# Optimization experiments

Hardware: AMD Instinct MI355X
Metric: run time of the kernel (lower is better)

## Reference

```python
import jax, jax.numpy as jnp
import numpy as np

B, S, D, H = 2, 2048, 1024, 16
HD = D // H  # head_dim = 64
NEG = -1.0e9


def setup_inputs() -> dict:
    key = jax.random.key(0)
    ks = jax.random.split(key, 9)
    s = 1.0 / np.sqrt(D)
    return {
        "x": jax.random.normal(ks[0], (B, S, D), jnp.float32),
        "mask": jnp.ones((B, S), jnp.float32),
        "Wq": jax.random.normal(ks[1], (D, D), jnp.float32) * s,
        "bq": jnp.zeros((D,), jnp.float32),
        "Wk": jax.random.normal(ks[2], (D, D), jnp.float32) * s,
        "bk": jnp.zeros((D,), jnp.float32),
        "Wv": jax.random.normal(ks[3], (D, D), jnp.float32) * s,
        "bv": jnp.zeros((D,), jnp.float32),
        "Wo": jax.random.normal(ks[4], (D, D), jnp.float32) * s,
        "bo": jnp.zeros((D,), jnp.float32),
    }


def reference(x, mask, Wq, bq, Wk, bk, Wv, bv, Wo, bo):
    # QKV projections -> [B, H, S, HD]
    def proj(t, W, b):
        return (t @ W + b).reshape(B, S, H, HD).transpose(0, 2, 1, 3)

    q = proj(x, Wq, bq)
    k = proj(x, Wk, bk)
    v = proj(x, Wv, bv)

    scores = jnp.einsum("bhqd,bhkd->bhqk", q, k) / jnp.sqrt(jnp.asarray(HD, x.dtype))
    # causal mask: scores * m + (1-m) * -1e9 (matches original exactly)
    cm = jnp.tril(jnp.ones((S, S), x.dtype))[None, None]
    scores = scores * cm + (1.0 - cm) * NEG
    # 2D padding mask branch
    scores = scores + (1.0 - mask[:, None, None, :]) * NEG

    attn = jax.nn.softmax(scores, axis=-1)
    out = jnp.einsum("bhqk,bhkd->bqhd", attn, v).reshape(B, S, D)
    return out @ Wo + bo
```

## Files before the change

kernel.cpp:

```cpp
#include <hip/hip_runtime.h>
#include <hip/hip_bf16.h>
#include <cstdint>
#include <cstddef>

typedef __attribute__((ext_vector_type(8))) short short8;
typedef __attribute__((ext_vector_type(4))) float floatx4;
typedef __attribute__((ext_vector_type(2))) unsigned int uintx2;

#define MFMA16(a, b, c) __builtin_amdgcn_mfma_f32_16x16x32_bf16((a), (b), (c), 0, 0, 0)
#define LOG2E 1.44269504088896340736f
#define EXP2(x) __builtin_amdgcn_exp2f(x)

__device__ __forceinline__ unsigned short f2bf(float f) {
  unsigned int u = __builtin_bit_cast(unsigned int, f);
  u += 0x7fffu + ((u >> 16) & 1u);
  return (unsigned short)(u >> 16);
}

__device__ __forceinline__ unsigned int pk2(float a, float b) {
  float2 f; f.x = a; f.y = b;
  __hip_bfloat162 h = __float22bfloat162_rn(f);
  unsigned int u;
  __builtin_memcpy(&u, &h, 4);
  return u;
}

typedef __attribute__((address_space(1))) void gvoid_t;
typedef __attribute__((address_space(3))) void svoid_t;
__device__ __forceinline__ void gload_lds16(const void* g, void* l) {
  __builtin_amdgcn_global_load_lds((gvoid_t*)(uintptr_t)g, (svoid_t*)(uintptr_t)l, 16, 0, 0);
}

__global__ void convert_x(const float* __restrict__ x, unsigned short* __restrict__ xb) {
  int i = (blockIdx.x * 256 + threadIdx.x) * 4;
  floatx4 v = *(const floatx4*)(x + i);
  uintx2 o;
  o[0] = pk2(v[0], v[1]);
  o[1] = pk2(v[2], v[3]);
  *(uintx2*)(xb + i) = o;
}

__global__ void transpose_w(const float* __restrict__ Wq, const float* __restrict__ Wk,
                            const float* __restrict__ Wv, const float* __restrict__ Wo,
                            unsigned short* __restrict__ Wqkvt, unsigned short* __restrict__ Wot) {
  __shared__ float tile[32][33];
  int z = blockIdx.z;
  const float* W = (z == 0) ? Wq : (z == 1) ? Wk : (z == 2) ? Wv : Wo;
  unsigned short* out = (z == 3) ? Wot : (Wqkvt + (size_t)z * 1024 * 1024);
  int n0 = blockIdx.x * 32, k0 = blockIdx.y * 32;
  int tx = threadIdx.x, ty = threadIdx.y;
#pragma unroll
  for (int j = 0; j < 4; ++j)
    tile[ty + j * 8][tx] = W[(size_t)(k0 + ty + j * 8) * 1024 + n0 + tx];
  __syncthreads();
#pragma unroll
  for (int j = 0; j < 4; ++j)
    out[(size_t)(n0 + ty + j * 8) * 1024 + k0 + tx] = f2bf(tile[tx][ty + j * 8]);
}

#define GEMM_PROLOGUE()                                                        \
  __shared__ __align__(16) unsigned short As[128 * 64];                        \
  __shared__ __align__(16) unsigned short Bs[128 * 64];                        \
  const int tid = threadIdx.x;                                                 \
  const int lane = tid & 63;                                                   \
  const int wid = tid >> 6;                                                    \
  const int col = lane & 15;                                                   \
  const int quad = lane >> 4;                                                  \
  const int m0 = blockIdx.x * 128;                                             \
  const int n0 = blockIdx.y * 128;                                             \
  const int wm = wid >> 1;                                                     \
  const int wn = wid & 1;                                                      \
  floatx4 acc[4][4];                                                           \
  _Pragma("unroll") for (int i = 0; i < 4; ++i)                                \
      _Pragma("unroll") for (int j = 0; j < 4; ++j)                            \
          acc[i][j] = (floatx4)(0.f);                                          \
  _Pragma("unroll 1") for (int kt = 0; kt < 16; ++kt) {                        \
    __syncthreads();                                                           \
    _Pragma("unroll") for (int call = 0; call < 4; ++call) {                   \
      int c = call * 256 + tid;                                                \
      int r = c >> 3, ch = c & 7;                                              \
      gload_lds16(A + (size_t)(m0 + r) * 1024 + kt * 64 + ((ch ^ (r & 7)) * 8),\
                  As + (size_t)(call * 256 + wid * 64) * 8);                   \
      gload_lds16(Bt + (size_t)(n0 + r) * 1024 + kt * 64 + ((ch ^ (r & 7)) * 8),\
                  Bs + (size_t)(call * 256 + wid * 64) * 8);                   \
    }                                                                          \
    __syncthreads();                                                           \
    _Pragma("unroll") for (int ks = 0; ks < 2; ++ks) {                         \
      short8 af[4], bf[4];                                                     \
      _Pragma("unroll") for (int rt = 0; rt < 4; ++rt) {                       \
        int row = wm * 64 + rt * 16 + col;                                     \
        af[rt] = *(const short8*)&As[row * 64 + (((ks * 4 + quad) ^ (row & 7)) * 8)]; \
      }                                                                        \
      _Pragma("unroll") for (int ct = 0; ct < 4; ++ct) {                       \
        int row = wn * 64 + ct * 16 + col;                                     \
        bf[ct] = *(const short8*)&Bs[row * 64 + (((ks * 4 + quad) ^ (row & 7)) * 8)]; \
      }                                                                        \
      _Pragma("unroll") for (int rt = 0; rt < 4; ++rt)                         \
          _Pragma("unroll") for (int ct = 0; ct < 4; ++ct)                     \
              acc[rt][ct] = MFMA16(af[rt], bf[ct], acc[rt][ct]);               \
    }                                                                          \
  }

__global__ __launch_bounds__(256, 3)
void gemm_qkv(const unsigned short* __restrict__ A, const unsigned short* __restrict__ Bt,
              const float* __restrict__ bq, const float* __restrict__ bk,
              const float* __restrict__ bv,
              unsigned short* __restrict__ Qo, unsigned short* __restrict__ Ko,
              unsigned short* __restrict__ Vo) {
  GEMM_PROLOGUE()
  const int nseg = n0 >> 10;
  const float* bias = (nseg == 0) ? bq : ((nseg == 1) ? bk : bv);
#pragma unroll
  for (int rt = 0; rt < 4; ++rt) {
#pragma unroll
    for (int ct = 0; ct < 4; ++ct) {
      int mg = m0 + wm * 64 + rt * 16 + quad * 4;
      int ng = n0 + wn * 64 + ct * 16 + col;
      int c = ng & 1023;
      int hh = c >> 6, hd = c & 63;
      int b_ = mg >> 11, s = mg & 2047;
      float bb = bias[c];
      if (nseg == 2) {
        uintx2 pk;
        pk[0] = pk2(acc[rt][ct][0] + bb, acc[rt][ct][1] + bb);
        pk[1] = pk2(acc[rt][ct][2] + bb, acc[rt][ct][3] + bb);
        *(uintx2*)&Vo[(size_t)(b_ * 16 + hh) * 131072 + (size_t)hd * 2048 + s] = pk;
      } else {
        unsigned short* dst =
            ((nseg == 0) ? Qo : Ko) + ((size_t)(b_ * 16 + hh) * 2048 + s) * 64 + hd;
        float scl = (nseg == 0) ? (0.125f * LOG2E) : 1.0f;
#pragma unroll
        for (int i = 0; i < 4; ++i) dst[(size_t)i * 64] = f2bf((acc[rt][ct][i] + bb) * scl);
      }
    }
  }
}

__global__ __launch_bounds__(256, 3)
void gemm_out(const unsigned short* __restrict__ A, const unsigned short* __restrict__ Bt,
              const float* __restrict__ bo, float* __restrict__ Out) {
  GEMM_PROLOGUE()
#pragma unroll
  for (int rt = 0; rt < 4; ++rt) {
#pragma unroll
    for (int ct = 0; ct < 4; ++ct) {
      int mg = m0 + wm * 64 + rt * 16 + quad * 4;
      int ng = n0 + wn * 64 + ct * 16 + col;
      float bb = bo[ng];
#pragma unroll
      for (int i = 0; i < 4; ++i)
        Out[(size_t)(mg + i) * 1024 + ng] = acc[rt][ct][i] + bb;
    }
  }
}

__global__ __launch_bounds__(256, 4)
void flash_attn(const unsigned short* __restrict__ Q, const unsigned short* __restrict__ K,
                const unsigned short* __restrict__ Vt, const float* __restrict__ mask,
                unsigned short* __restrict__ O) {
  __shared__ __align__(16) unsigned short Ks[128 * 64];
  __shared__ __align__(16) unsigned short Vs[64 * 128];

  const int tid = threadIdx.x;
  const int lane = tid & 63;
  const int wid = tid >> 6;
  const int col = lane & 15;
  const int quad = lane >> 4;
  const int slot = (int)(blockIdx.x >> 8);
  const int g = (int)(blockIdx.x & 255);
  const int h8 = g >> 5;
  const int bh = g & 31;
  const int j = (slot == 0) ? (31 - h8) : (slot == 1) ? h8 : (slot == 2) ? (23 - h8) : (8 + h8);
  const int b = bh >> 4, h = bh & 15;
  const int q0 = j * 64;
  const int tdiag = j >> 1;

  const unsigned short* Qp = Q + (size_t)bh * 2048 * 64;
  const unsigned short* Kp = K + (size_t)bh * 2048 * 64;
  const unsigned short* Vp = Vt + (size_t)bh * 64 * 2048;
  const float* mp = mask + b * 2048;

  const int lr8 = lane >> 3, lc8 = lane & 7;
  const int lr16 = lane >> 4, lc16 = lane & 15;
  const floatx4 fzero = (floatx4)(0.f);
  const floatx4 fone = (floatx4)(1.f);

#pragma unroll
  for (int i = 0; i < 2; ++i) {
    int seg = wid * 2 + i;
    int r = seg * 8 + lr8;
    gload_lds16(Qp + (size_t)(q0 + r) * 64 + ((lc8 ^ (r & 7)) * 8), Ks + seg * 512);
  }
  __syncthreads();
  short8 qf[2];
  {
    int q = wid * 16 + col;
#pragma unroll
    for (int ks = 0; ks < 2; ++ks)
      qf[ks] = *(const short8*)&Ks[q * 64 + (((ks * 4 + quad) ^ (q & 7)) * 8)];
  }
  unsigned int mbits = 0;
  for (int t = 0; t <= tdiag; ++t) {
    float2 mv = *(const float2*)&mp[t * 128 + lane * 2];
    unsigned long long bb = __ballot(mv.x != 1.f || mv.y != 1.f);
    mbits |= (bb ? 1u : 0u) << t;
  }

  floatx4 o[4];
#pragma unroll
  for (int dt = 0; dt < 4; ++dt) o[dt] = fzero;
  float mrow = -1e30f;
  float lrow = 0.f;

#pragma unroll 1
  for (int t = 0; t <= tdiag; ++t) {
    __syncthreads();
#pragma unroll
    for (int i = 0; i < 4; ++i) {
      int seg = wid * 4 + i;
      int r = seg * 8 + lr8;
      gload_lds16(Kp + (size_t)(t * 128 + r) * 64 + ((lc8 ^ (r & 7)) * 8), Ks + seg * 512);
    }
#pragma unroll
    for (int i = 0; i < 4; ++i) {
      int seg = wid * 4 + i;
      int r = seg * 4 + lr16;
      gload_lds16(Vp + (size_t)r * 2048 + t * 128 + ((lc16 ^ (r & 15)) * 8), Vs + seg * 512);
    }
    __syncthreads();

    floatx4 sc[8];
    __builtin_amdgcn_s_setprio(1);
#pragma unroll
    for (int rt = 0; rt < 8; ++rt) {
      int kr = rt * 16 + col;
      short8 kf0 = *(const short8*)&Ks[kr * 64 + ((quad ^ (col & 7)) * 8)];
      short8 kf1 = *(const short8*)&Ks[kr * 64 + (((4 + quad) ^ (col & 7)) * 8)];
      floatx4 s0 = MFMA16(kf0, qf[0], fzero);
      sc[rt] = MFMA16(kf1, qf[1], s0);
    }
    __builtin_amdgcn_s_setprio(0);
    __syncthreads();

    if (__builtin_amdgcn_readfirstlane(mbits >> t) & 1) {
#pragma unroll
      for (int rt = 0; rt < 8; ++rt) {
        floatx4 mm = *(const floatx4*)&mp[t * 128 + rt * 16 + quad * 4];
        sc[rt] += (fone - mm) * (-1.0e9f * LOG2E);
      }
    }
    if (t == tdiag) {
      int qg = q0 + wid * 16 + col;
#pragma unroll
      for (int rt = 0; rt < 8; ++rt)
#pragma unroll
        for (int i = 0; i < 4; ++i)
          if (t * 128 + rt * 16 + quad * 4 + i > qg) sc[rt][i] = -1.0e9f * LOG2E;
    }

    float mt = -1e30f;
#pragma unroll
    for (int rt = 0; rt < 8; ++rt)
      mt = fmaxf(mt, fmaxf(fmaxf(sc[rt][0], sc[rt][1]), fmaxf(sc[rt][2], sc[rt][3])));
    mt = fmaxf(mt, __shfl_xor(mt, 16));
    mt = fmaxf(mt, __shfl_xor(mt, 32));

    const bool skip = (__all(mt - mrow <= 8.0f) != 0);
    float mn = mrow;
    if (!skip) {
      mn = fmaxf(mrow, mt);
      float alpha = EXP2(mrow - mn);
      mrow = mn;
      lrow *= alpha;
#pragma unroll
      for (int dt = 0; dt < 4; ++dt) o[dt] *= alpha;
    }
    float sum = 0.f;
#pragma unroll
    for (int rt = 0; rt < 8; ++rt)
#pragma unroll
      for (int i = 0; i < 4; ++i) {
        float p = EXP2(sc[rt][i] - mn);
        sc[rt][i] = p;
        sum += p;
      }
    sum += __shfl_xor(sum, 16);
    sum += __shfl_xor(sum, 32);
    lrow += sum;

    {
      int qloc = wid * 16 + col;
#pragma unroll
      for (int rt = 0; rt < 8; ++rt) {
        uintx2 w;
        w[0] = pk2(sc[rt][0], sc[rt][1]);
        w[1] = pk2(sc[rt][2], sc[rt][3]);
        int chunk = (rt * 2 + (quad >> 1)) ^ col;
        *(uintx2*)&Ks[qloc * 128 + chunk * 8 + (quad & 1) * 4] = w;
      }
    }
    __builtin_amdgcn_s_setprio(1);
#pragma unroll
    for (int ks = 0; ks < 4; ++ks) {
      int ch = ks * 4 + quad;
      short8 pf = *(const short8*)&Ks[(wid * 16 + col) * 128 + ((ch ^ col) * 8)];
#pragma unroll
      for (int dt = 0; dt < 4; ++dt) {
        short8 vf = *(const short8*)&Vs[(dt * 16 + col) * 128 + ((ch ^ col) * 8)];
        o[dt] = MFMA16(vf, pf, o[dt]);
      }
    }
    __builtin_amdgcn_s_setprio(0);
  }

  {
    float inv = 1.0f / lrow;
    int qg = q0 + wid * 16 + col;
    unsigned short* dst = O + ((size_t)(b * 2048 + qg)) * 1024 + h * 64;
#pragma unroll
    for (int dt = 0; dt < 4; ++dt) {
      uintx2 pk;
      pk[0] = pk2(o[dt][0] * inv, o[dt][1] * inv);
      pk[1] = pk2(o[dt][2] * inv, o[dt][3] * inv);
      *(uintx2*)&dst[dt * 16 + quad * 4] = pk;
    }
  }
}

extern "C" void kernel_launch(void* const* d_in, const int* in_sizes, int n_in,
                              void* d_out, int out_size, void* d_ws, size_t ws_size,
                              hipStream_t stream) {
  (void)in_sizes; (void)n_in; (void)out_size; (void)ws_size;
  const float* x  = (const float*)d_in[0];
  const float* mask = (const float*)d_in[1];
  const float* Wq = (const float*)d_in[2];
  const float* bq = (const float*)d_in[3];
  const float* Wk = (const float*)d_in[4];
  const float* bk = (const float*)d_in[5];
  const float* Wv = (const float*)d_in[6];
  const float* bv = (const float*)d_in[7];
  const float* Wo = (const float*)d_in[8];
  const float* bo = (const float*)d_in[9];
  float* out = (float*)d_out;

  char* ws = (char*)d_ws;
  unsigned short* xb    = (unsigned short*)(ws);
  unsigned short* Wqkvt = (unsigned short*)(ws + (8u << 20));
  unsigned short* Wot   = (unsigned short*)(ws + (14u << 20));
  unsigned short* Qb    = (unsigned short*)(ws + (16u << 20));
  unsigned short* Kb    = (unsigned short*)(ws + (24u << 20));
  unsigned short* Vtb   = (unsigned short*)(ws + (32u << 20));
  unsigned short* Ao    = (unsigned short*)(ws + (40u << 20));

  convert_x<<<4096, 256, 0, stream>>>(x, xb);
  transpose_w<<<dim3(32, 32, 4), dim3(32, 8), 0, stream>>>(Wq, Wk, Wv, Wo, Wqkvt, Wot);
  gemm_qkv<<<dim3(32, 24), 256, 0, stream>>>(xb, Wqkvt, bq, bk, bv, Qb, Kb, Vtb);
  flash_attn<<<dim3(1024), 256, 0, stream>>>(Qb, Kb, Vtb, mask, Ao);
  gemm_out<<<dim3(32, 8), 256, 0, stream>>>(Ao, Wot, bo, out);
}
```

Before: 183.6 us.

## Split KV range for long causal query tiles and merge partials in a combine kernel

Query tiles in the upper half of the sequence (j ≥ 16) are now processed by two blocks, each covering half of the causal KV range. Each block writes a normalized bf16 partial output plus its row max and row sum to workspace. A new combine kernel rescales and merges the two partials into the attention output, while the shorter tiles still write directly. The aim is to shrink the longest per-block work so the tail of the attention grid is shorter and better balanced across CUs. The cost is an extra kernel launch, an extra bf16 rounding of the partials, and more global traffic for the partial outputs and statistics.

```diff
diff --git a/kernel.cpp b/kernel.cpp
--- a/kernel.cpp
+++ b/kernel.cpp
@@ -6,6 +6,7 @@
 typedef __attribute__((ext_vector_type(8))) short short8;
 typedef __attribute__((ext_vector_type(4))) float floatx4;
 typedef __attribute__((ext_vector_type(2))) unsigned int uintx2;
+typedef __attribute__((ext_vector_type(4))) unsigned int uintx4;
 
 #define MFMA16(a, b, c) __builtin_amdgcn_mfma_f32_16x16x32_bf16((a), (b), (c), 0, 0, 0)
 #define LOG2E 1.44269504088896340736f
@@ -15,6 +16,11 @@
   unsigned int u = __builtin_bit_cast(unsigned int, f);
   u += 0x7fffu + ((u >> 16) & 1u);
   return (unsigned short)(u >> 16);
+}
+
+__device__ __forceinline__ float bf2f(unsigned short u) {
+  unsigned int x = (unsigned int)u << 16;
+  return __builtin_bit_cast(float, x);
 }
 
 __device__ __forceinline__ unsigned int pk2(float a, float b) {
@@ -157,7 +163,9 @@
 __global__ __launch_bounds__(256, 4)
 void flash_attn(const unsigned short* __restrict__ Q, const unsigned short* __restrict__ K,
                 const unsigned short* __restrict__ Vt, const float* __restrict__ mask,
-                unsigned short* __restrict__ O) {
+                unsigned short* __restrict__ O,
+                unsigned short* __restrict__ P0, unsigned short* __restrict__ P1,
+                float* __restrict__ mlm, float* __restrict__ mll) {
   __shared__ __align__(16) unsigned short Ks[128 * 64];
   __shared__ __align__(16) unsigned short Vs[64 * 128];
 
@@ -166,11 +174,17 @@
   const int wid = tid >> 6;
   const int col = lane & 15;
   const int quad = lane >> 4;
-  const int slot = (int)(blockIdx.x >> 8);
-  const int g = (int)(blockIdx.x & 255);
-  const int h8 = g >> 5;
-  const int bh = g & 31;
-  const int j = (slot == 0) ? (31 - h8) : (slot == 1) ? h8 : (slot == 2) ? (23 - h8) : (8 + h8);
+
+  const int id = (int)blockIdx.x;
+  int j, t0, t1, split, u;
+  if (id < 512) {
+    u = id; j = 31 - (u >> 5); int nt = (j >> 1) + 1; t0 = nt >> 1; t1 = nt; split = 1;
+  } else if (id < 1024) {
+    u = id - 512; j = 31 - (u >> 5); int nt = (j >> 1) + 1; t0 = 0; t1 = nt >> 1; split = 0;
+  } else {
+    u = id - 1024; j = 15 - (u >> 5); t0 = 0; t1 = (j >> 1) + 1; split = -1;
+  }
+  const int bh = u & 31;
   const int b = bh >> 4, h = bh & 15;
   const int q0 = j * 64;
   const int tdiag = j >> 1;
@@ -200,7 +214,7 @@
       qf[ks] = *(const short8*)&Ks[q * 64 + (((ks * 4 + quad) ^ (q & 7)) * 8)];
   }
   unsigned int mbits = 0;
-  for (int t = 0; t <= tdiag; ++t) {
+  for (int t = t0; t < t1; ++t) {
     float2 mv = *(const float2*)&mp[t * 128 + lane * 2];
     unsigned long long bb = __ballot(mv.x != 1.f || mv.y != 1.f);
     mbits |= (bb ? 1u : 0u) << t;
@@ -213,7 +227,7 @@
   float lrow = 0.f;
 
 #pragma unroll 1
-  for (int t = 0; t <= tdiag; ++t) {
+  for (int t = t0; t < t1; ++t) {
     __syncthreads();
 #pragma unroll
     for (int i = 0; i < 4; ++i) {
@@ -313,8 +327,8 @@
     __builtin_amdgcn_s_setprio(0);
   }
 
-  {
-    float inv = 1.0f / lrow;
+  float inv = 1.0f / lrow;
+  if (split < 0) {
     int qg = q0 + wid * 16 + col;
     unsigned short* dst = O + ((size_t)(b * 2048 + qg)) * 1024 + h * 64;
 #pragma unroll
@@ -324,7 +338,52 @@
       pk[1] = pk2(o[dt][2] * inv, o[dt][3] * inv);
       *(uintx2*)&dst[dt * 16 + quad * 4] = pk;
     }
-  }
+  } else {
+    int tidx = (j - 16) * 32 + bh;
+    int q = wid * 16 + col;
+    unsigned short* dst = (split ? P1 : P0) + (size_t)tidx * 4096 + q * 64;
+#pragma unroll
+    for (int dt = 0; dt < 4; ++dt) {
+      uintx2 pk;
+      pk[0] = pk2(o[dt][0] * inv, o[dt][1] * inv);
+      pk[1] = pk2(o[dt][2] * inv, o[dt][3] * inv);
+      *(uintx2*)&dst[dt * 16 + quad * 4] = pk;
+    }
+    if (quad == 0) {
+      mlm[split * 32768 + tidx * 64 + q] = mrow;
+      mll[split * 32768 + tidx * 64 + q] = lrow;
+    }
+  }
+}
+
+__global__ __launch_bounds__(256)
+void combine(const unsigned short* __restrict__ P0, const unsigned short* __restrict__ P1,
+             const float* __restrict__ mlm, const float* __restrict__ mll,
+             unsigned short* __restrict__ O) {
+  int gid = blockIdx.x * 256 + threadIdx.x;
+  int row = gid >> 3;
+  int d0 = (gid & 7) * 8;
+  int tile = row >> 6, q = row & 63;
+  int j = 16 + (tile >> 5), bh = tile & 31;
+  int b = bh >> 4, h = bh & 15;
+  float m0 = mlm[tile * 64 + q], m1 = mlm[32768 + tile * 64 + q];
+  float l0 = mll[tile * 64 + q], l1 = mll[32768 + tile * 64 + q];
+  float m = fmaxf(m0, m1);
+  float w0 = l0 * EXP2(m0 - m), w1 = l1 * EXP2(m1 - m);
+  float inv = 1.0f / (w0 + w1);
+  w0 *= inv; w1 *= inv;
+  short8 a = *(const short8*)&P0[(size_t)tile * 4096 + q * 64 + d0];
+  short8 c = *(const short8*)&P1[(size_t)tile * 4096 + q * 64 + d0];
+  int s = j * 64 + q;
+  unsigned short* dst = O + ((size_t)(b * 2048 + s)) * 1024 + h * 64 + d0;
+  uintx4 pk;
+#pragma unroll
+  for (int i = 0; i < 4; ++i) {
+    float e0 = bf2f((unsigned short)a[2 * i]) * w0 + bf2f((unsigned short)c[2 * i]) * w1;
+    float e1 = bf2f((unsigned short)a[2 * i + 1]) * w0 + bf2f((unsigned short)c[2 * i + 1]) * w1;
+    pk[i] = pk2(e0, e1);
+  }
+  *(uintx4*)dst = pk;
 }
 
 extern "C" void kernel_launch(void* const* d_in, const int* in_sizes, int n_in,
@@ -351,10 +410,15 @@
   unsigned short* Kb    = (unsigned short*)(ws + (24u << 20));
   unsigned short* Vtb   = (unsigned short*)(ws + (32u << 20));
   unsigned short* Ao    = (unsigned short*)(ws + (40u << 20));
+  unsigned short* P0    = (unsigned short*)(ws);
+  unsigned short* P1    = (unsigned short*)(ws + (4u << 20));
+  float*          mlm   = (float*)(ws + (8u << 20));
+  float*          mll   = (float*)(ws + (8u << 20) + (1u << 18));
 
   convert_x<<<4096, 256, 0, stream>>>(x, xb);
   transpose_w<<<dim3(32, 32, 4), dim3(32, 8), 0, stream>>>(Wq, Wk, Wv, Wo, Wqkvt, Wot);
   gemm_qkv<<<dim3(32, 24), 256, 0, stream>>>(xb, Wqkvt, bq, bk, bv, Qb, Kb, Vtb);
-  flash_attn<<<dim3(1024), 256, 0, stream>>>(Qb, Kb, Vtb, mask, Ao);
+  flash_attn<<<dim3(1536), 256, 0, stream>>>(Qb, Kb, Vtb, mask, Ao, P0, P1, mlm, mll);
+  combine<<<dim3(1024), 256, 0, stream>>>(P0, P1, mlm, mll, Ao);
   gemm_out<<<dim3(32, 8), 256, 0, stream>>>(Ao, Wot, bo, out);
 }
```

Result: slower. 188.4 us (+2.6%).

## Double-buffer K/V tiles in flash attention and simplify block scheduling

Applied to the files above, without the earlier changes.

Flash attention now uses two LDS buffers, prefetching the next K/V tile while computing on the current one instead of loading synchronously each iteration. LDS use doubles to 64KB, so launch bounds drop from 4 to 2 blocks per CU. The block-to-query-tile mapping changes from the interleaved four-slot balancing scheme to a simple descending order by tile index. The aim is to hide global load latency, at the cost of lower occupancy and a different load-balancing order.

```diff
diff --git a/kernel.cpp b/kernel.cpp
--- a/kernel.cpp
+++ b/kernel.cpp
@@ -154,26 +154,23 @@
   }
 }
 
-__global__ __launch_bounds__(256, 4)
+__global__ __launch_bounds__(256, 2)
 void flash_attn(const unsigned short* __restrict__ Q, const unsigned short* __restrict__ K,
                 const unsigned short* __restrict__ Vt, const float* __restrict__ mask,
                 unsigned short* __restrict__ O) {
-  __shared__ __align__(16) unsigned short Ks[128 * 64];
-  __shared__ __align__(16) unsigned short Vs[64 * 128];
+  __shared__ __align__(16) unsigned short SB[2][16384];
 
   const int tid = threadIdx.x;
   const int lane = tid & 63;
   const int wid = tid >> 6;
   const int col = lane & 15;
   const int quad = lane >> 4;
-  const int slot = (int)(blockIdx.x >> 8);
-  const int g = (int)(blockIdx.x & 255);
-  const int h8 = g >> 5;
-  const int bh = g & 31;
-  const int j = (slot == 0) ? (31 - h8) : (slot == 1) ? h8 : (slot == 2) ? (23 - h8) : (8 + h8);
+  const int j = 31 - (int)(blockIdx.x >> 5);
+  const int bh = blockIdx.x & 31;
   const int b = bh >> 4, h = bh & 15;
   const int q0 = j * 64;
   const int tdiag = j >> 1;
+  const int nt = tdiag + 1;
 
   const unsigned short* Qp = Q + (size_t)bh * 2048 * 64;
   const unsigned short* Kp = K + (size_t)bh * 2048 * 64;
@@ -189,7 +186,7 @@
   for (int i = 0; i < 2; ++i) {
     int seg = wid * 2 + i;
     int r = seg * 8 + lr8;
-    gload_lds16(Qp + (size_t)(q0 + r) * 64 + ((lc8 ^ (r & 7)) * 8), Ks + seg * 512);
+    gload_lds16(Qp + (size_t)(q0 + r) * 64 + ((lc8 ^ (r & 7)) * 8), &SB[0][seg * 512]);
   }
   __syncthreads();
   short8 qf[2];
@@ -197,14 +194,29 @@
     int q = wid * 16 + col;
 #pragma unroll
     for (int ks = 0; ks < 2; ++ks)
-      qf[ks] = *(const short8*)&Ks[q * 64 + (((ks * 4 + quad) ^ (q & 7)) * 8)];
+      qf[ks] = *(const short8*)&SB[0][q * 64 + (((ks * 4 + quad) ^ (q & 7)) * 8)];
   }
   unsigned int mbits = 0;
-  for (int t = 0; t <= tdiag; ++t) {
+  for (int t = 0; t < nt; ++t) {
     float2 mv = *(const float2*)&mp[t * 128 + lane * 2];
     unsigned long long bb = __ballot(mv.x != 1.f || mv.y != 1.f);
     mbits |= (bb ? 1u : 0u) << t;
   }
+  __syncthreads();
+
+#pragma unroll
+  for (int i = 0; i < 4; ++i) {
+    int seg = wid * 4 + i;
+    int r = seg * 8 + lr8;
+    gload_lds16(Kp + (size_t)r * 64 + ((lc8 ^ (r & 7)) * 8), &SB[0][seg * 512]);
+  }
+#pragma unroll
+  for (int i = 0; i < 4; ++i) {
+    int seg = wid * 4 + i;
+    int r = seg * 4 + lr16;
+    gload_lds16(Vp + (size_t)r * 2048 + ((lc16 ^ (r & 15)) * 8), &SB[0][8192 + seg * 512]);
+  }
+  __syncthreads();
 
   floatx4 o[4];
 #pragma unroll
@@ -213,34 +225,43 @@
   float lrow = 0.f;
 
 #pragma unroll 1
-  for (int t = 0; t <= tdiag; ++t) {
-    __syncthreads();
-#pragma unroll
-    for (int i = 0; i < 4; ++i) {
-      int seg = wid * 4 + i;
-      int r = seg * 8 + lr8;
-      gload_lds16(Kp + (size_t)(t * 128 + r) * 64 + ((lc8 ^ (r & 7)) * 8), Ks + seg * 512);
-    }
-#pragma unroll
-    for (int i = 0; i < 4; ++i) {
-      int seg = wid * 4 + i;
-      int r = seg * 4 + lr16;
-      gload_lds16(Vp + (size_t)r * 2048 + t * 128 + ((lc16 ^ (r & 15)) * 8), Vs + seg * 512);
-    }
-    __syncthreads();
+  for (int t = 0; t < nt; ++t) {
+    const int cur = t & 1;
+    unsigned short* Ksb = &SB[cur][0];
+    unsigned short* Vsb = &SB[cur][8192];
+
+    if (t + 1 < nt) {
+      unsigned short* Kn = &SB[cur ^ 1][0];
+      unsigned short* Vn = &SB[cur ^ 1][8192];
+#pragma unroll
+      for (int i = 0; i < 4; ++i) {
+        int seg = wid * 4 + i;
+        int r = seg * 8 + lr8;
+        gload_lds16(Kp + (size_t)((t + 1) * 128 + r) * 64 + ((lc8 ^ (r & 7)) * 8),
+                    Kn + seg * 512);
+      }
+#pragma unroll
+      for (int i = 0; i < 4; ++i) {
+        int seg = wid * 4 + i;
+        int r = seg * 4 + lr16;
+        gload_lds16(Vp + (size_t)r * 2048 + (t + 1) * 128 + ((lc16 ^ (r & 15)) * 8),
+                    Vn + seg * 512);
+      }
+    }
 
     floatx4 sc[8];
     __builtin_amdgcn_s_setprio(1);
 #pragma unroll
     for (int rt = 0; rt < 8; ++rt) {
       int kr = rt * 16 + col;
-      short8 kf0 = *(const short8*)&Ks[kr * 64 + ((quad ^ (col & 7)) * 8)];
-      short8 kf1 = *(const short8*)&Ks[kr * 64 + (((4 + quad) ^ (col & 7)) * 8)];
+      short8 kf0 = *(const short8*)&Ksb[kr * 64 + ((quad ^ (col & 7)) * 8)];
+      short8 kf1 = *(const short8*)&Ksb[kr * 64 + (((4 + quad) ^ (col & 7)) * 8)];
       floatx4 s0 = MFMA16(kf0, qf[0], fzero);
       sc[rt] = MFMA16(kf1, qf[1], s0);
     }
     __builtin_amdgcn_s_setprio(0);
-    __syncthreads();
+    asm volatile("s_waitcnt lgkmcnt(0)" ::: "memory");
+    __builtin_amdgcn_s_barrier();
 
     if (__builtin_amdgcn_readfirstlane(mbits >> t) & 1) {
 #pragma unroll
@@ -296,21 +317,23 @@
         w[0] = pk2(sc[rt][0], sc[rt][1]);
         w[1] = pk2(sc[rt][2], sc[rt][3]);
         int chunk = (rt * 2 + (quad >> 1)) ^ col;
-        *(uintx2*)&Ks[qloc * 128 + chunk * 8 + (quad & 1) * 4] = w;
+        *(uintx2*)&Ksb[qloc * 128 + chunk * 8 + (quad & 1) * 4] = w;
       }
     }
     __builtin_amdgcn_s_setprio(1);
 #pragma unroll
     for (int ks = 0; ks < 4; ++ks) {
       int ch = ks * 4 + quad;
-      short8 pf = *(const short8*)&Ks[(wid * 16 + col) * 128 + ((ch ^ col) * 8)];
+      short8 pf = *(const short8*)&Ksb[(wid * 16 + col) * 128 + ((ch ^ col) * 8)];
 #pragma unroll
       for (int dt = 0; dt < 4; ++dt) {
-        short8 vf = *(const short8*)&Vs[(dt * 16 + col) * 128 + ((ch ^ col) * 8)];
+        short8 vf = *(const short8*)&Vsb[(dt * 16 + col) * 128 + ((ch ^ col) * 8)];
         o[dt] = MFMA16(vf, pf, o[dt]);
       }
     }
     __builtin_amdgcn_s_setprio(0);
+
+    __syncthreads();
   }
 
   {
```

Result: slower. 188.5 us (+2.7%).
